# Kernel tuning notes

Hardware: AMD Instinct MI355X
Metric: run time of the kernel (lower is better)

The kernel has to match this reference:

```python
import jax, jax.numpy as jnp
import numpy as np

S = 7          # grid_size
B = 2          # num_boxes
C = 80         # num_classes
LC = 5.0       # lambda_coord
LN = 0.5       # lambda_noobj
BT = 8192      # batch
N = 32         # gt boxes per image (distinct cells)


def setup_inputs() -> dict:
    key = jax.random.key(0)
    kp, kc, ko, kw, kl = jax.random.split(key, 5)
    preds = jax.random.normal(kp, (BT, S, S, B * 5 + C), jnp.float32)
    # choose N distinct grid cells per image so scatter-set is deterministic
    cells = jnp.argsort(jax.random.uniform(kc, (BT, S * S)), axis=-1)[:, :N]
    gi = cells % S
    gj = cells // S
    off = jax.random.uniform(ko, (BT, N, 2), minval=0.05, maxval=0.95)
    cx = (gi.astype(jnp.float32) + off[..., 0]) / S
    cy = (gj.astype(jnp.float32) + off[..., 1]) / S
    wh = jax.random.uniform(kw, (BT, N, 2), minval=0.05, maxval=0.3)
    gt_boxes = jnp.stack([cx - 0.5 * wh[..., 0], cy - 0.5 * wh[..., 1],
                          cx + 0.5 * wh[..., 0], cy + 0.5 * wh[..., 1]], axis=-1)
    gt_labels = jax.random.randint(kl, (BT, N), 0, C)
    gt_valid = jnp.ones((BT, N), dtype=bool)
    return {"preds": preds, "gt_boxes": gt_boxes,
            "gt_labels": gt_labels, "gt_valid": gt_valid}


def reference(preds, gt_boxes, gt_labels, gt_valid):
    Bt = preds.shape[0]
    dt = preds.dtype
    pred_cls = preds[..., B * 5:]                              # [Bt,S,S,C]
    pb = preds[..., :B * 5].reshape(Bt, S, S, B, 5)            # [Bt,S,S,B,5]

    x1, y1, x2, y2 = (gt_boxes[..., i] for i in range(4))      # each [Bt,N]
    cx = (x1 + x2) * 0.5
    cy = (y1 + y2) * 0.5
    w = jnp.maximum(x2 - x1, 1e-6)
    h = jnp.maximum(y2 - y1, 1e-6)
    gi = jnp.clip(jnp.floor(cx * S), 0, S - 1).astype(jnp.int32)
    gj = jnp.clip(jnp.floor(cy * S), 0, S - 1).astype(jnp.int32)

    bidx = jnp.arange(Bt, dtype=jnp.int32)[:, None]
    cell = pb[bidx, gj, gi]                                    # [Bt,N,B,5]

    # decode predicted boxes for the matched cell
    px = (jax.nn.sigmoid(cell[..., 0]) + gi[..., None].astype(dt)) / S
    py = (jax.nn.sigmoid(cell[..., 1]) + gj[..., None].astype(dt)) / S
    pw = cell[..., 2] ** 2
    ph = cell[..., 3] ** 2
    px1 = px - 0.5 * pw; py1 = py - 0.5 * ph
    px2 = px + 0.5 * pw; py2 = py + 0.5 * ph

    # IoU of B predicted boxes vs the gt box, vectorized over [Bt,N]
    gx1 = x1[..., None]; gy1 = y1[..., None]
    gx2 = x2[..., None]; gy2 = y2[..., None]
    iw = jnp.clip(jnp.minimum(px2, gx2) - jnp.maximum(px1, gx1), 0.0)
    ih = jnp.clip(jnp.minimum(py2, gy2) - jnp.maximum(py1, gy1), 0.0)
    inter = iw * ih
    area_p = (px2 - px1) * (py2 - py1)
    area_g = ((x2 - x1) * (y2 - y1))[..., None]
    ious = inter / (area_p + area_g - inter + 1e-6)            # [Bt,N,B]

    best = jnp.argmax(ious, axis=-1)                           # [Bt,N]
    iou_best = jax.lax.stop_gradient(
        jnp.take_along_axis(ious, best[..., None], axis=-1)[..., 0])

    # scatter target assignment (distinct cells -> deterministic set)
    flat_pb = Bt * S * S * B
    idx = ((bidx * S + gj) * S + gi) * B + best.astype(jnp.int32)
    idx = jnp.where(gt_valid, idx, flat_pb)                    # OOB -> dropped
    obj = jnp.zeros(flat_pb, bool).at[idx].set(True, mode='drop').reshape(Bt, S, S, B)
    conf_t = jnp.zeros(flat_pb, dt).at[idx].set(iou_best, mode='drop').reshape(Bt, S, S, B)
    tgt = jnp.stack([cx * S - gi.astype(dt), cy * S - gj.astype(dt),
                     jnp.sqrt(w), jnp.sqrt(h)], axis=-1)       # [Bt,N,4]
    coord_t = jnp.zeros((flat_pb, 4), dt).at[idx].set(tgt, mode='drop').reshape(Bt, S, S, B, 4)
    flat_c = Bt * S * S * C
    cidx = ((bidx * S + gj) * S + gi) * C + gt_labels.astype(jnp.int32)
    cidx = jnp.where(gt_valid, cidx, flat_c)
    cls_t = jnp.zeros(flat_c, dt).at[cidx].set(1.0, mode='drop').reshape(Bt, S, S, C)

    # masked MSE reductions
    pm = obj.astype(dt)
    nm = 1.0 - pm
    cm = obj.any(axis=-1).astype(dt)
    n_pos = jnp.maximum(pm.sum(), 1.0)
    n_neg = jnp.maximum(nm.sum(), 1.0)
    n_cell = jnp.maximum(cm.sum(), 1.0)

    sx = jax.nn.sigmoid(pb[..., 0])
    sy = jax.nn.sigmoid(pb[..., 1])
    so = jax.nn.sigmoid(pb[..., 4])
    loss_x = (pm * (sx - coord_t[..., 0]) ** 2).sum()
    loss_y = (pm * (sy - coord_t[..., 1]) ** 2).sum()
    loss_w = (pm * (pb[..., 2] - coord_t[..., 2]) ** 2).sum()
    loss_h = (pm * (pb[..., 3] - coord_t[..., 3]) ** 2).sum()
    loss_coord = LC * (loss_x + loss_y + loss_w + loss_h) / n_pos
    loss_obj = (pm * (so - conf_t) ** 2).sum() / n_pos
    loss_noobj = LN * (nm * (so - conf_t) ** 2).sum() / n_neg
    sp = jax.nn.softmax(pred_cls, axis=-1)
    loss_cls = (cm * ((sp - cls_t) ** 2).sum(axis=-1)).sum() / n_cell
    return loss_coord + loss_obj + loss_noobj + loss_cls
```

## Files before the change

kernel.cpp:

```cpp
#include <hip/hip_runtime.h>

#define S7 7
#define NCH 90
#define NCELL 49
#define NGT 32
#define STRIDE 91

__device__ __forceinline__ float sigm(float x) { return 1.0f / (1.0f + __expf(-x)); }

__global__ __launch_bounds__(256) void yolo_fused(
    const float*  __restrict__ preds,
    const float4* __restrict__ gt_boxes,
    const int*    __restrict__ gt_labels,
    float* __restrict__ ws,
    float c_coord, float c_obj, float c_noobj, float c_cls)
{
    __shared__ float s_rows[NGT * STRIDE];
    __shared__ int   s_cell[NGT];
    __shared__ int   s_lab[NGT];
    __shared__ float s_red[4];

    const int t = threadIdx.x;
    const int b = blockIdx.x;
    const float* img = preds + (size_t)b * NCELL * NCH;

    float conf_v = 0.f;
    if (t < 2 * NCELL) conf_v = img[(t >> 1) * NCH + 4 + 5 * (t & 1)];

    float gif = 0.f, gjf = 0.f, x1 = 0.f, y1 = 0.f, x2 = 0.f, y2 = 0.f;
    float tx = 0.f, ty = 0.f, sw = 0.f, sh = 0.f, ag = 0.f;
    if (t < NGT) {
        float4 g = gt_boxes[(size_t)b * NGT + t];
        x1 = g.x; y1 = g.y; x2 = g.z; y2 = g.w;
        float cx = (x1 + x2) * 0.5f, cy = (y1 + y2) * 0.5f;
        float w = fmaxf(x2 - x1, 1e-6f), h = fmaxf(y2 - y1, 1e-6f);
        gif = fminf(fmaxf(floorf(cx * 7.f), 0.f), 6.f);
        gjf = fminf(fmaxf(floorf(cy * 7.f), 0.f), 6.f);
        tx = cx * 7.f - gif;  ty = cy * 7.f - gjf;
        sw = sqrtf(w);        sh = sqrtf(h);
        ag = (x2 - x1) * (y2 - y1);
        s_cell[t] = (int)gjf * S7 + (int)gif;
        s_lab[t]  = gt_labels[(size_t)b * NGT + t];
    }
    __syncthreads();

    for (int i = t; i < NGT * NCH; i += 256) {
        int r  = i / NCH;
        int ch = i - r * NCH;
        s_rows[r * STRIDE + ch] = img[s_cell[r] * NCH + ch];
    }
    __syncthreads();

    float part = 0.f;

    if (t < 2 * NCELL) {
        float so = sigm(conf_v);
        part += c_noobj * so * so;
    }

    if (t < NGT) {
        float c[10];
        #pragma unroll
        for (int k = 0; k < 10; ++k) c[k] = s_rows[t * STRIDE + k];
        float iou[2];
        #pragma unroll
        for (int bb = 0; bb < 2; ++bb) {
            float px = (sigm(c[bb * 5 + 0]) + gif) / 7.f;
            float py = (sigm(c[bb * 5 + 1]) + gjf) / 7.f;
            float pw = c[bb * 5 + 2] * c[bb * 5 + 2];
            float ph = c[bb * 5 + 3] * c[bb * 5 + 3];
            float px1 = px - 0.5f * pw, px2 = px + 0.5f * pw;
            float py1 = py - 0.5f * ph, py2 = py + 0.5f * ph;
            float iw = fmaxf(fminf(px2, x2) - fmaxf(px1, x1), 0.f);
            float ih = fmaxf(fminf(py2, y2) - fmaxf(py1, y1), 0.f);
            float inter = iw * ih;
            float ap = (px2 - px1) * (py2 - py1);
            iou[bb] = inter / (ap + ag - inter + 1e-6f);
        }
        int best = (iou[1] > iou[0]) ? 1 : 0;
        float ioub = iou[best];
        float soB  = sigm(c[best * 5 + 4]);
        part += c_obj * (soB - ioub) * (soB - ioub);
        part -= c_noobj * soB * soB;
        float sx = sigm(c[best * 5 + 0]), sy = sigm(c[best * 5 + 1]);
        float dx = sx - tx, dy = sy - ty;
        float dw = c[best * 5 + 2] - sw, dh = c[best * 5 + 3] - sh;
        part += c_coord * (dx * dx + dy * dy + dw * dw + dh * dh);
    }

    {
        int g = t >> 3, u = t & 7;
        int lab = s_lab[g];
        float s = 0.f, q = 0.f, el = 0.f;
        int base = g * STRIDE + 10 + u * 10;
        #pragma unroll
        for (int k = 0; k < 10; ++k) {
            float e = __expf(s_rows[base + k]);
            s += e;
            q = fmaf(e, e, q);
            el = (u * 10 + k == lab) ? e : el;
        }
        #pragma unroll
        for (int off = 1; off <= 4; off <<= 1) {
            s  += __shfl_xor(s,  off, 64);
            q  += __shfl_xor(q,  off, 64);
            el += __shfl_xor(el, off, 64);
        }
        if (u == 0) {
            float inv = 1.f / s;
            part += c_cls * fmaf(q * inv, inv, fmaf(-2.f * el, inv, 1.f));
        }
    }

    #pragma unroll
    for (int off = 32; off >= 1; off >>= 1) part += __shfl_xor(part, off, 64);
    if ((t & 63) == 0) s_red[t >> 6] = part;
    __syncthreads();
    if (t == 0) ws[b] = s_red[0] + s_red[1] + s_red[2] + s_red[3];
}

__global__ __launch_bounds__(256) void yolo_reduce(const float* __restrict__ ws,
                                                   float* __restrict__ out, int n) {
    float v = 0.f;
    for (int i = threadIdx.x; i < n; i += 256) v += ws[i];
    #pragma unroll
    for (int off = 32; off >= 1; off >>= 1) v += __shfl_xor(v, off, 64);
    __shared__ float r[4];
    if ((threadIdx.x & 63) == 0) r[threadIdx.x >> 6] = v;
    __syncthreads();
    if (threadIdx.x == 0) out[0] = r[0] + r[1] + r[2] + r[3];
}

extern "C" void kernel_launch(void* const* d_in, const int* in_sizes, int n_in,
                              void* d_out, int out_size, void* d_ws, size_t ws_size,
                              hipStream_t stream)
{
    const float*  preds     = (const float*)d_in[0];
    const float4* gt_boxes  = (const float4*)d_in[1];
    const int*    gt_labels = (const int*)d_in[2];
    int Bt = in_sizes[0] / (NCELL * NCH);

    float n_pos = (float)Bt * NGT;
    float n_neg = (float)Bt * (2 * NCELL - NGT);
    float c_coord = 5.0f / n_pos;
    float c_obj   = 1.0f / n_pos;
    float c_noobj = 0.5f / n_neg;
    float c_cls   = 1.0f / n_pos;

    float* ws = (float*)d_ws;
    yolo_fused<<<dim3(Bt), dim3(256), 0, stream>>>(preds, gt_boxes, gt_labels, ws,
                                                   c_coord, c_obj, c_noobj, c_cls);
    yolo_reduce<<<dim3(1), dim3(256), 0, stream>>>(ws, (float*)d_out, Bt);
}
```

Baseline: 229.9 us.

## Gather matched cell rows directly from global memory, drop shared staging

Result: faster. 218.4 us (-5.0%).

```diff
diff --git a/kernel.cpp b/kernel.cpp
--- a/kernel.cpp
+++ b/kernel.cpp
@@ -4,7 +4,6 @@
 #define NCH 90
 #define NCELL 49
 #define NGT 32
-#define STRIDE 91
 
 __device__ __forceinline__ float sigm(float x) { return 1.0f / (1.0f + __expf(-x)); }
 
@@ -15,11 +14,6 @@
     float* __restrict__ ws,
     float c_coord, float c_obj, float c_noobj, float c_cls)
 {
-    __shared__ float s_rows[NGT * STRIDE];
-    __shared__ int   s_cell[NGT];
-    __shared__ int   s_lab[NGT];
-    __shared__ float s_red[4];
-
     const int t = threadIdx.x;
     const int b = blockIdx.x;
     const float* img = preds + (size_t)b * NCELL * NCH;
@@ -27,29 +21,23 @@
     float conf_v = 0.f;
     if (t < 2 * NCELL) conf_v = img[(t >> 1) * NCH + 4 + 5 * (t & 1)];
 
-    float gif = 0.f, gjf = 0.f, x1 = 0.f, y1 = 0.f, x2 = 0.f, y2 = 0.f;
-    float tx = 0.f, ty = 0.f, sw = 0.f, sh = 0.f, ag = 0.f;
-    if (t < NGT) {
-        float4 g = gt_boxes[(size_t)b * NGT + t];
-        x1 = g.x; y1 = g.y; x2 = g.z; y2 = g.w;
-        float cx = (x1 + x2) * 0.5f, cy = (y1 + y2) * 0.5f;
-        float w = fmaxf(x2 - x1, 1e-6f), h = fmaxf(y2 - y1, 1e-6f);
-        gif = fminf(fmaxf(floorf(cx * 7.f), 0.f), 6.f);
-        gjf = fminf(fmaxf(floorf(cy * 7.f), 0.f), 6.f);
-        tx = cx * 7.f - gif;  ty = cy * 7.f - gjf;
-        sw = sqrtf(w);        sh = sqrtf(h);
-        ag = (x2 - x1) * (y2 - y1);
-        s_cell[t] = (int)gjf * S7 + (int)gif;
-        s_lab[t]  = gt_labels[(size_t)b * NGT + t];
-    }
-    __syncthreads();
+    const int g = t >> 3, u = t & 7;
+    const int n = b * NGT + g;
+    float4 gb = gt_boxes[n];
+    int lab = gt_labels[n];
 
-    for (int i = t; i < NGT * NCH; i += 256) {
-        int r  = i / NCH;
-        int ch = i - r * NCH;
-        s_rows[r * STRIDE + ch] = img[s_cell[r] * NCH + ch];
-    }
-    __syncthreads();
+    float x1 = gb.x, y1 = gb.y, x2 = gb.z, y2 = gb.w;
+    float cx = (x1 + x2) * 0.5f, cy = (y1 + y2) * 0.5f;
+    float gif = fminf(fmaxf(floorf(cx * 7.f), 0.f), 6.f);
+    float gjf = fminf(fmaxf(floorf(cy * 7.f), 0.f), 6.f);
+    int cell = (int)gjf * S7 + (int)gif;
+    const float2* row2 = (const float2*)(img + cell * NCH);
+
+    float2 cv0 = row2[5 + 5 * u];
+    float2 cv1 = row2[6 + 5 * u];
+    float2 cv2 = row2[7 + 5 * u];
+    float2 cv3 = row2[8 + 5 * u];
+    float2 cv4 = row2[9 + 5 * u];
 
     float part = 0.f;
 
@@ -58,10 +46,36 @@
         part += c_noobj * so * so;
     }
 
-    if (t < NGT) {
-        float c[10];
+    float s = 0.f, q = 0.f, el = 0.f;
+    {
+        float2 cv[5] = {cv0, cv1, cv2, cv3, cv4};
         #pragma unroll
-        for (int k = 0; k < 10; ++k) c[k] = s_rows[t * STRIDE + k];
+        for (int k = 0; k < 5; ++k) {
+            float e0 = __expf(cv[k].x);
+            float e1 = __expf(cv[k].y);
+            int cid = 10 * u + 2 * k;
+            s += e0 + e1;
+            q = fmaf(e0, e0, q);
+            q = fmaf(e1, e1, q);
+            el = (cid     == lab) ? e0 : el;
+            el = (cid + 1 == lab) ? e1 : el;
+        }
+        #pragma unroll
+        for (int off = 1; off <= 4; off <<= 1) {
+            s  += __shfl_xor(s,  off, 64);
+            q  += __shfl_xor(q,  off, 64);
+            el += __shfl_xor(el, off, 64);
+        }
+    }
+
+    if (u == 0) {
+        float inv = 1.f / s;
+        part += c_cls * fmaf(q * inv, inv, fmaf(-2.f * el, inv, 1.f));
+
+        float2 b0 = row2[0], b1 = row2[1], b2 = row2[2], b3 = row2[3], b4 = row2[4];
+        float c[10] = {b0.x, b0.y, b1.x, b1.y, b2.x, b2.y, b3.x, b3.y, b4.x, b4.y};
+        float w = fmaxf(x2 - x1, 1e-6f), h = fmaxf(y2 - y1, 1e-6f);
+        float ag = (x2 - x1) * (y2 - y1);
         float iou[2];
         #pragma unroll
         for (int bb = 0; bb < 2; ++bb) {
@@ -82,38 +96,16 @@
         float soB  = sigm(c[best * 5 + 4]);
         part += c_obj * (soB - ioub) * (soB - ioub);
         part -= c_noobj * soB * soB;
+        float tx = cx * 7.f - gif, ty = cy * 7.f - gjf;
         float sx = sigm(c[best * 5 + 0]), sy = sigm(c[best * 5 + 1]);
         float dx = sx - tx, dy = sy - ty;
-        float dw = c[best * 5 + 2] - sw, dh = c[best * 5 + 3] - sh;
+        float dw = c[best * 5 + 2] - sqrtf(w), dh = c[best * 5 + 3] - sqrtf(h);
         part += c_coord * (dx * dx + dy * dy + dw * dw + dh * dh);
-    }
-
-    {
-        int g = t >> 3, u = t & 7;
-        int lab = s_lab[g];
-        float s = 0.f, q = 0.f, el = 0.f;
-        int base = g * STRIDE + 10 + u * 10;
-        #pragma unroll
-        for (int k = 0; k < 10; ++k) {
-            float e = __expf(s_rows[base + k]);
-            s += e;
-            q = fmaf(e, e, q);
-            el = (u * 10 + k == lab) ? e : el;
-        }
-        #pragma unroll
-        for (int off = 1; off <= 4; off <<= 1) {
-            s  += __shfl_xor(s,  off, 64);
-            q  += __shfl_xor(q,  off, 64);
-            el += __shfl_xor(el, off, 64);
-        }
-        if (u == 0) {
-            float inv = 1.f / s;
-            part += c_cls * fmaf(q * inv, inv, fmaf(-2.f * el, inv, 1.f));
-        }
     }
 
     #pragma unroll
     for (int off = 32; off >= 1; off >>= 1) part += __shfl_xor(part, off, 64);
+    __shared__ float s_red[4];
     if ((t & 63) == 0) s_red[t >> 6] = part;
     __syncthreads();
     if (t == 0) ws[b] = s_red[0] + s_red[1] + s_red[2] + s_red[3];
```
